# Kernel tuning notes

Measured on AMD Instinct MI355X. Metric: run time of the kernel, lower is better.

The kernel has to match this reference:

```python
import jax, jax.numpy as jnp
import numpy as np
from jax import lax

G, N0, E, P = 50, 1000, 4000, 10          # graphs, nodes/graph, edges/graph, patients
FEAT, NHID, GDIM, RATIO = 1036, 128, 32, 0.2
NLAYERS = 3


def setup_inputs():
    key = jax.random.key(0)
    ks = jax.random.split(key, 32)
    x = jax.random.uniform(ks[0], (G * N0, FEAT), jnp.float32)
    off = (jnp.arange(G) * N0)[:, None]
    src = jax.random.randint(ks[1], (G, E), 0, N0) + off
    dst = jax.random.randint(ks[2], (G, E), 0, N0) + off
    edge_index = jnp.stack([src.reshape(-1), dst.reshape(-1)]).astype(jnp.int32)
    graphs_per_pat = jnp.full((P,), G // P, jnp.int32)

    def lin(k, i, o):
        return jax.random.normal(k, (i, o), jnp.float32) / np.float32(np.sqrt(i))

    d = {"x": x, "edge_index": edge_index, "graphs_per_pat": graphs_per_pat}
    ins = [FEAT, NHID, NHID]
    ki = 3
    for l in range(NLAYERS):
        d[f"c{l}_wl"] = lin(ks[ki], ins[l], NHID)
        d[f"c{l}_bl"] = jnp.zeros(NHID, jnp.float32)
        d[f"c{l}_wr"] = lin(ks[ki + 1], ins[l], NHID)
        d[f"p{l}_wrel"] = lin(ks[ki + 2], NHID, 1)
        d[f"p{l}_brel"] = jnp.zeros(1, jnp.float32)
        d[f"p{l}_wroot"] = lin(ks[ki + 3], NHID, 1)
        ki += 4
    d["lin1_w"] = lin(ks[ki], 2 * NHID, NHID); d["lin1_b"] = jnp.zeros(NHID, jnp.float32)
    d["lin2_w"] = lin(ks[ki + 1], NHID, GDIM); d["lin2_b"] = jnp.zeros(GDIM, jnp.float32)
    d["grade_w"] = lin(ks[ki + 2], GDIM, 3); d["grade_b"] = jnp.zeros(3, jnp.float32)
    d["haz_w"] = lin(ks[ki + 3], GDIM, 1); d["haz_b"] = jnp.zeros(1, jnp.float32)
    return d


def _sage(x, src, dst, m, wl, bl, wr, M):
    # PyG SAGEConv, mean aggregation: out = lin_l(mean_j x_j) + lin_r(x_i)
    agg = jax.ops.segment_sum(x[src] * m[:, None], dst, num_segments=M)
    cnt = jax.ops.segment_sum(m, dst, num_segments=M)
    mean = agg / jnp.maximum(cnt, 1.0)[:, None]
    return mean @ wl + bl + x @ wr


def _sag_pool(x, src, dst, m, wrel, brel, wroot, n, k):
    # SAGPooling: GraphConv (add aggr) score -> per-graph top-k -> tanh gate -> edge filter
    M = G * n
    agg = jax.ops.segment_sum(x[src] * m[:, None], dst, num_segments=M)
    score = (agg @ wrel + brel + x @ wroot).reshape(G, n)  # [G, n]
    _, idx = lax.top_k(score, k)                            # [G, k]
    sel = jnp.take_along_axis(score, idx, axis=1)           # [G, k]
    perm = (idx + (jnp.arange(G) * n)[:, None]).reshape(-1)
    nx = x[perm] * jnp.tanh(sel).reshape(-1, 1)             # [G*k, NHID]
    mapping = jnp.full((M,), -1, jnp.int32).at[perm].set(jnp.arange(G * k, dtype=jnp.int32))
    ns, nd = mapping[src], mapping[dst]
    nm = m * (ns >= 0) * (nd >= 0)                          # keep edge iff both endpoints survive
    return nx, jnp.maximum(ns, 0), jnp.maximum(nd, 0), nm


def _forward(x, edge_index, graphs_per_pat, params):
    # normalize_graphs: first 12 feature columns divided by their column max
    x = jnp.concatenate([x[:, :12] / jnp.max(x[:, :12], axis=0, keepdims=True), x[:, 12:]], axis=1)
    src, dst = edge_index[0], edge_index[1]
    m = jnp.ones(src.shape[0], x.dtype)
    n = N0
    xs = []
    for l in range(NLAYERS):
        k = int(np.ceil(RATIO * n))
        x = jax.nn.relu(_sage(x, src, dst, m, params[f"c{l}_wl"], params[f"c{l}_bl"], params[f"c{l}_wr"], G * n))
        x, src, dst, m = _sag_pool(x, src, dst, m, params[f"p{l}_wrel"], params[f"p{l}_brel"], params[f"p{l}_wroot"], n, k)
        n = k
        xr = x.reshape(G, n, NHID)
        xs.append(jnp.concatenate([xr.max(axis=1), xr.mean(axis=1)], axis=1))  # [G, 2*NHID]
    h = xs[0] + xs[1] + xs[2]
    # patient-level mean pool
    bv = jnp.repeat(jnp.arange(P), graphs_per_pat, total_repeat_length=G)
    pooled = jax.ops.segment_sum(h, bv, num_segments=P) / graphs_per_pat[:, None].astype(h.dtype)
    h = jax.nn.relu(pooled @ params["lin1_w"] + params["lin1_b"])  # dropout omitted (deterministic ref)
    feats = jax.nn.relu(h @ params["lin2_w"] + params["lin2_b"])
    grade = jax.nn.log_softmax(feats @ params["grade_w"] + params["grade_b"], axis=1)
    hazard = jax.nn.sigmoid(feats @ params["haz_w"] + params["haz_b"]) * 6.0 - 3.0
    return feats, grade, hazard


def reference(x, edge_index, graphs_per_pat,
              c0_wl, c0_bl, c0_wr, p0_wrel, p0_brel, p0_wroot,
              c1_wl, c1_bl, c1_wr, p1_wrel, p1_brel, p1_wroot,
              c2_wl, c2_bl, c2_wr, p2_wrel, p2_brel, p2_wroot,
              lin1_w, lin1_b, lin2_w, lin2_b, grade_w, grade_b, haz_w, haz_b):
    params = dict(
        c0_wl=c0_wl, c0_bl=c0_bl, c0_wr=c0_wr, p0_wrel=p0_wrel, p0_brel=p0_brel, p0_wroot=p0_wroot,
        c1_wl=c1_wl, c1_bl=c1_bl, c1_wr=c1_wr, p1_wrel=p1_wrel, p1_brel=p1_brel, p1_wroot=p1_wroot,
        c2_wl=c2_wl, c2_bl=c2_bl, c2_wr=c2_wr, p2_wrel=p2_wrel, p2_brel=p2_brel, p2_wroot=p2_wroot,
        lin1_w=lin1_w, lin1_b=lin1_b, lin2_w=lin2_w, lin2_b=lin2_b,
        grade_w=grade_w, grade_b=grade_b, haz_w=haz_w, haz_b=haz_b)
    return _forward(x, edge_index, graphs_per_pat, params)
```

## Files before the change

### kernel.cpp

```cpp
#include <hip/hip_runtime.h>
#include <math.h>
#include <cfloat>

#define G_    50
#define N0_   1000
#define NEDGE 200000
#define EPG_  (NEDGE/G_)
#define P_    10
#define FEAT_ 1036
#define NHID_ 128
#define GDIM_ 32
#define K0_   200
#define K1_   40
#define K2_   8
#define M0_   (G_*N0_)
#define M1_   (G_*K0_)
#define M2_   (G_*K1_)

#define KPAD_ 1088
#define MPAD0_ 50048
#define MPAD1_ 10112
#define MPAD2_ 2048

typedef __attribute__((ext_vector_type(8))) short s16x8;
typedef __attribute__((ext_vector_type(4))) float f32x4;

__device__ __forceinline__ unsigned f2bf1(float f) {
  unsigned u = __float_as_uint(f);
  return (u + 0x7FFFu + ((u >> 16) & 1u)) >> 16;
}
__device__ __forceinline__ unsigned packbf(float a, float b) {
  return f2bf1(a) | (f2bf1(b) << 16);
}

__device__ __forceinline__ void gload_lds16(const void* g, void* l) {
  __builtin_amdgcn_global_load_lds((const __attribute__((address_space(1))) void*)g,
                                   (__attribute__((address_space(3))) void*)l, 16, 0, 0);
}


__global__ void colmax_kernel(const float* __restrict__ x, int* __restrict__ scale_i) {
  int tid = threadIdx.x, wave = tid >> 6, lane = tid & 63;
  float mx[12];
#pragma unroll
  for (int j = 0; j < 12; j++) mx[j] = 0.f;
  for (int r = blockIdx.x * 256 + tid; r < M0_; r += gridDim.x * 256) {
    const float4* p = (const float4*)(x + (size_t)r * FEAT_);
    float4 a = p[0], b = p[1], c = p[2];
    mx[0] = fmaxf(mx[0], a.x); mx[1] = fmaxf(mx[1], a.y);
    mx[2] = fmaxf(mx[2], a.z); mx[3] = fmaxf(mx[3], a.w);
    mx[4] = fmaxf(mx[4], b.x); mx[5] = fmaxf(mx[5], b.y);
    mx[6] = fmaxf(mx[6], b.z); mx[7] = fmaxf(mx[7], b.w);
    mx[8] = fmaxf(mx[8], c.x); mx[9] = fmaxf(mx[9], c.y);
    mx[10] = fmaxf(mx[10], c.z); mx[11] = fmaxf(mx[11], c.w);
  }
#pragma unroll
  for (int off = 32; off > 0; off >>= 1)
#pragma unroll
    for (int j = 0; j < 12; j++) mx[j] = fmaxf(mx[j], __shfl_down(mx[j], off));
  __shared__ float red[4][12];
  if (lane == 0)
#pragma unroll
    for (int j = 0; j < 12; j++) red[wave][j] = mx[j];
  __syncthreads();
  if (tid < 12) {
    float m = fmaxf(fmaxf(red[0][tid], red[1][tid]), fmaxf(red[2][tid], red[3][tid]));
    atomicMax(scale_i + tid, __float_as_int(m));
  }
}

__global__ void build_wt0_kernel(const float* __restrict__ wl, const float* __restrict__ wr,
                                 const int* __restrict__ scale_i, unsigned short* __restrict__ WT) {
  int idx = blockIdx.x * blockDim.x + threadIdx.x;
  if (idx >= 256 * KPAD_) return;
  int c = idx / KPAD_, j = idx % KPAD_;
  float w = 0.f;
  if (j < FEAT_) {
    w = (c < NHID_) ? wl[j * NHID_ + c] : wr[j * NHID_ + (c - NHID_)];
    if (j < 12) w *= 1.0f / __int_as_float(scale_i[j]);
  }
  WT[idx] = (unsigned short)f2bf1(w);
}

__global__ void build_wt12_kernel(const float* __restrict__ wl1, const float* __restrict__ wr1,
                                  const float* __restrict__ wl2, const float* __restrict__ wr2,
                                  unsigned short* __restrict__ WTA, unsigned short* __restrict__ WTB) {
  int idx = blockIdx.x * blockDim.x + threadIdx.x;
  if (idx >= 2 * 256 * 128) return;
  int l = idx >> 15, r = idx & 32767;
  int c = r >> 7, j = r & 127;
  const float* wl = l ? wl2 : wl1;
  const float* wr = l ? wr2 : wr1;
  float w = (c < NHID_) ? wl[j * NHID_ + c] : wr[j * NHID_ + (c - NHID_)];
  (l ? WTB : WTA)[r] = (unsigned short)f2bf1(w);
}

template <bool AF32>
__global__ __launch_bounds__(256) void mfma_gemm_kernel(const float* __restrict__ Af,
                                                        const unsigned short* __restrict__ Ab,
                                                        const unsigned short* __restrict__ WT,
                                                        float* __restrict__ C, int M,
                                                        int lda, int ldb, int kvalid, int ksteps) {
  __shared__ unsigned short As[2 * 128 * 32];
  __shared__ unsigned short Bs[2 * 256 * 32];
  const int bm = blockIdx.x * 128;
  const int tid = threadIdx.x, wave = tid >> 6, lane = tid & 63;
  const int wr = wave >> 1, wc = wave & 1;
  const int lhi = lane >> 4, llo = lane & 15;
  const int arow = tid >> 1, ahalf = tid & 1;
  f32x4 acc[4][8] = {};

  for (int st = 0; st < ksteps; st++) {
    const int k0 = st * 64;
#pragma unroll
    for (int it = 0; it < 8; it++) {
      int c = it * 256 + wave * 64 + lane;
      int kk = c >> 10, r = (c >> 2) & 255, cb = c & 3;
      gload_lds16(WT + (size_t)r * ldb + k0 + kk * 32 + cb * 8, Bs + (size_t)c * 8);
    }
    {
      int gr = bm + arow;
      int gk = k0 + ahalf * 32;
      unsigned short* dstp = As + ahalf * 4096 + arow * 32;
      if (AF32) {
        float f[32];
        if (gr < M && gk + 32 <= kvalid) {
          const float4* ap = (const float4*)(Af + (size_t)gr * lda + gk);
#pragma unroll
          for (int j = 0; j < 8; j++) {
            float4 v = ap[j];
            f[4 * j] = v.x; f[4 * j + 1] = v.y; f[4 * j + 2] = v.z; f[4 * j + 3] = v.w;
          }
        } else {
          const float* ap = Af + (size_t)gr * lda + gk;
#pragma unroll
          for (int j = 0; j < 32; j++)
            f[j] = (gr < M && gk + j < kvalid) ? ap[j] : 0.f;
        }
#pragma unroll
        for (int j = 0; j < 4; j++) {
          uint4 p;
          p.x = packbf(f[8 * j + 0], f[8 * j + 1]); p.y = packbf(f[8 * j + 2], f[8 * j + 3]);
          p.z = packbf(f[8 * j + 4], f[8 * j + 5]); p.w = packbf(f[8 * j + 6], f[8 * j + 7]);
          *(uint4*)(dstp + j * 8) = p;
        }
      } else {
        const uint4* ap = (const uint4*)(Ab + (size_t)gr * lda + gk);
#pragma unroll
        for (int j = 0; j < 4; j++) ((uint4*)dstp)[j] = ap[j];
      }
    }
    __syncthreads();

#pragma unroll
    for (int kk = 0; kk < 2; kk++) {
      s16x8 a[4], b[8];
#pragma unroll
      for (int mt = 0; mt < 4; mt++)
        a[mt] = *(const s16x8*)&As[kk * 4096 + (wr * 64 + mt * 16 + llo) * 32 + lhi * 8];
#pragma unroll
      for (int nt = 0; nt < 8; nt++)
        b[nt] = *(const s16x8*)&Bs[kk * 8192 + (wc * 128 + nt * 16 + llo) * 32 + lhi * 8];
#pragma unroll
      for (int mt = 0; mt < 4; mt++)
#pragma unroll
        for (int nt = 0; nt < 8; nt++)
          acc[mt][nt] = __builtin_amdgcn_mfma_f32_16x16x32_bf16(a[mt], b[nt], acc[mt][nt], 0, 0, 0);
    }
    __syncthreads();
  }

#pragma unroll
  for (int mt = 0; mt < 4; mt++) {
#pragma unroll
    for (int q = 0; q < 4; q++) {
      int row = bm + wr * 64 + mt * 16 + lhi * 4 + q;
      if (row < M) {
#pragma unroll
        for (int nt = 0; nt < 8; nt++)
          C[(size_t)row * 256 + wc * 128 + nt * 16 + llo] = acc[mt][nt][q];
      }
    }
  }
}

__global__ __launch_bounds__(1024) void csr_graph_kernel(const int* __restrict__ src,
                                                         const int* __restrict__ dst,
                                                         const float* __restrict__ m, int n,
                                                         int* __restrict__ deg,
                                                         int* __restrict__ offs,
                                                         int* __restrict__ eid) {
  __shared__ int sdeg[1024];
  __shared__ int soff[1024];
  __shared__ int scur[1024];
  __shared__ int spart[1024];
  const int g = blockIdx.x, tid = threadIdx.x;
  sdeg[tid] = 0;
  __syncthreads();
  const int e0 = g * EPG_;
  for (int e = tid; e < EPG_; e += 1024) {
    int ge = e0 + e;
    if (!m || m[ge] != 0.f) atomicAdd(&sdeg[dst[ge] - g * n], 1);
  }
  __syncthreads();
  int v = (tid < n) ? sdeg[tid] : 0;
  spart[tid] = v;
  __syncthreads();
  for (int ofs = 1; ofs < 1024; ofs <<= 1) {
    int t = (tid >= ofs) ? spart[tid - ofs] : 0;
    __syncthreads();
    spart[tid] += t;
    __syncthreads();
  }
  if (tid < n) {
    soff[tid] = spart[tid] - sdeg[tid];
    scur[tid] = 0;
    deg[g * n + tid] = sdeg[tid];
    offs[g * n + tid] = g * EPG_ + soff[tid];
  }
  __syncthreads();
  for (int e = tid; e < EPG_; e += 1024) {
    int ge = e0 + e;
    if (!m || m[ge] != 0.f) {
      int d = dst[ge] - g * n;
      int p = atomicAdd(&scur[d], 1);
      eid[g * EPG_ + soff[d] + p] = src[ge];
    }
  }
}

__global__ void agg_sage_dots_kernel(const float* __restrict__ Y,
                                     const int* __restrict__ eid, const int* __restrict__ offs,
                                     const int* __restrict__ deg,
                                     const float* __restrict__ bl,
                                     const float* __restrict__ wrel, const float* __restrict__ wroot,
                                     float* __restrict__ X, float* __restrict__ T,
                                     float* __restrict__ R, int M) {
  int wid = threadIdx.x >> 6, lane = threadIdx.x & 63;
  int i = blockIdx.x * 4 + wid;
  if (i >= M) return;
  int d = deg[i], o = offs[i];
  float a0 = 0.f, a1 = 0.f;
  for (int j = 0; j < d; j++) {
    int s = eid[o + j];
    a0 += Y[(size_t)s * 256 + lane];
    a1 += Y[(size_t)s * 256 + 64 + lane];
  }
  float ic = 1.f / fmaxf((float)d, 1.f);
  float v0 = a0 * ic + bl[lane] + Y[(size_t)i * 256 + 128 + lane];
  float v1 = a1 * ic + bl[64 + lane] + Y[(size_t)i * 256 + 192 + lane];
  v0 = fmaxf(v0, 0.f); v1 = fmaxf(v1, 0.f);
  X[(size_t)i * 128 + lane] = v0;
  X[(size_t)i * 128 + 64 + lane] = v1;
  float t = v0 * wrel[lane] + v1 * wrel[64 + lane];
  float r = v0 * wroot[lane] + v1 * wroot[64 + lane];
#pragma unroll
  for (int off = 32; off > 0; off >>= 1) {
    t += __shfl_down(t, off);
    r += __shfl_down(r, off);
  }
  if (lane == 0) { T[i] = t; R[i] = r; }
}

template <int NP>
__global__ __launch_bounds__(1024) void pool_kernel(
    const float* __restrict__ X, const float* __restrict__ T, const float* __restrict__ R,
    const float* __restrict__ brel,
    const int* __restrict__ src, const int* __restrict__ dst, const float* __restrict__ m,
    const int* __restrict__ deg, const int* __restrict__ offs, const int* __restrict__ eid,
    int n, int k,
    unsigned short* __restrict__ NXB,
    int* __restrict__ nsrc, int* __restrict__ ndst, float* __restrict__ nm,
    float* __restrict__ H) {
  __shared__ float val[NP];
  __shared__ int   ind[256];
  __shared__ int   lmap[NP];
  __shared__ float gate[256];
  __shared__ float redmx[8][128];
  __shared__ float redsm[8][128];
  const int g = blockIdx.x, tid = threadIdx.x, nthr = blockDim.x;
  float b0 = brel[0];
  for (int i = tid; i < n; i += nthr) {
    int gi = g * n + i;
    int dd = deg[gi], o = offs[gi];
    float s = 0.f;
    for (int j = 0; j < dd; j++) s += T[eid[o + j]];
    val[i] = s + R[gi] + b0;
    lmap[i] = -1;
  }
  __syncthreads();
  for (int i = tid; i < n; i += nthr) {
    float vi = val[i];
    int rank = 0;
    for (int j = 0; j < n; j++) {
      float vj = val[j];
      rank += (vj > vi) || (vj == vi && j < i);
    }
    if (rank < k) {
      lmap[i] = rank;
      ind[rank] = i;
      gate[rank] = tanhf(vi);
    }
  }
  __syncthreads();
  for (int idx = tid; idx < k * 128; idx += nthr) {
    int t = idx >> 7, c = idx & 127;
    float v = X[(size_t)(g * n + ind[t]) * 128 + c] * gate[t];
    NXB[(size_t)(g * k + t) * 128 + c] = (unsigned short)f2bf1(v);
  }
  {
    int c = tid & 127, seg = tid >> 7;
    float mxv = -FLT_MAX, smv = 0.f;
    for (int t = seg; t < k; t += 8) {
      float v = X[(size_t)(g * n + ind[t]) * 128 + c] * gate[t];
      mxv = fmaxf(mxv, v);
      smv += v;
    }
    redmx[seg][c] = mxv;
    redsm[seg][c] = smv;
  }
  __syncthreads();
  if (tid < 128) {
    float Mv = redmx[0][tid], S = redsm[0][tid];
#pragma unroll
    for (int s2 = 1; s2 < 8; s2++) { Mv = fmaxf(Mv, redmx[s2][tid]); S += redsm[s2][tid]; }
    H[g * 256 + tid] += Mv;
    H[g * 256 + 128 + tid] += S / (float)k;
  }
  if (nsrc) {
    const int e0 = g * EPG_;
    for (int e = tid; e < EPG_; e += nthr) {
      int ge = e0 + e;
      int ls = lmap[src[ge] - g * n], ld = lmap[dst[ge] - g * n];
      float me = m ? m[ge] : 1.f;
      nm[ge] = (ls >= 0 && ld >= 0) ? me : 0.f;
      nsrc[ge] = g * k + max(ls, 0);
      ndst[ge] = g * k + max(ld, 0);
    }
  }
}

__global__ void head_kernel(const float* __restrict__ H, const int* __restrict__ gpp,
                            const float* __restrict__ lin1_w, const float* __restrict__ lin1_b,
                            const float* __restrict__ lin2_w, const float* __restrict__ lin2_b,
                            const float* __restrict__ grade_w, const float* __restrict__ grade_b,
                            const float* __restrict__ haz_w, const float* __restrict__ haz_b,
                            float* __restrict__ out) {
  __shared__ float pooled[P_][256];
  __shared__ float h1[P_][NHID_];
  __shared__ float feats[P_][GDIM_];
  __shared__ int off[P_ + 1];
  int tid = threadIdx.x;
  if (tid == 0) {
    off[0] = 0;
    for (int p = 0; p < P_; p++) off[p + 1] = min(off[p] + gpp[p], G_);
  }
  __syncthreads();
  for (int idx = tid; idx < P_ * 256; idx += blockDim.x) {
    int p = idx >> 8, c = idx & 255;
    int a = off[p], b = (p == P_ - 1) ? G_ : off[p + 1];
    float s = 0.f;
    for (int gq = a; gq < b; gq++) s += H[gq * 256 + c];
    pooled[p][c] = s / (float)gpp[p];
  }
  __syncthreads();
  for (int idx = tid; idx < P_ * NHID_; idx += blockDim.x) {
    int p = idx >> 7, o = idx & 127;
    float acc = lin1_b[o];
    for (int c = 0; c < 256; c++) acc += pooled[p][c] * lin1_w[c * NHID_ + o];
    h1[p][o] = fmaxf(acc, 0.f);
  }
  __syncthreads();
  for (int idx = tid; idx < P_ * GDIM_; idx += blockDim.x) {
    int p = idx / GDIM_, o = idx % GDIM_;
    float acc = lin2_b[o];
    for (int c = 0; c < NHID_; c++) acc += h1[p][c] * lin2_w[c * GDIM_ + o];
    float f = fmaxf(acc, 0.f);
    feats[p][o] = f;
    out[p * GDIM_ + o] = f;
  }
  __syncthreads();
  if (tid < P_) {
    int p = tid;
    float l[3];
    float mx = -FLT_MAX;
    for (int j = 0; j < 3; j++) {
      float acc = grade_b[j];
      for (int c = 0; c < GDIM_; c++) acc += feats[p][c] * grade_w[c * 3 + j];
      l[j] = acc;
      mx = fmaxf(mx, acc);
    }
    float se = 0.f;
    for (int j = 0; j < 3; j++) se += expf(l[j] - mx);
    float lse = mx + logf(se);
    for (int j = 0; j < 3; j++) out[P_ * GDIM_ + p * 3 + j] = l[j] - lse;
    float z = haz_b[0];
    for (int c = 0; c < GDIM_; c++) z += feats[p][c] * haz_w[c];
    out[P_ * GDIM_ + P_ * 3 + p] = 6.f / (1.f + expf(-z)) - 3.f;
  }
}

extern "C" void kernel_launch(void* const* d_in, const int* in_sizes, int n_in,
                              void* d_out, int out_size, void* d_ws, size_t ws_size,
                              hipStream_t stream) {
  (void)in_sizes; (void)n_in; (void)out_size; (void)ws_size;
  const float* x  = (const float*)d_in[0];
  const int* ei   = (const int*)d_in[1];
  const int* gpp  = (const int*)d_in[2];
  const float* c_wl[3]    = {(const float*)d_in[3],  (const float*)d_in[9],  (const float*)d_in[15]};
  const float* c_bl[3]    = {(const float*)d_in[4],  (const float*)d_in[10], (const float*)d_in[16]};
  const float* c_wr[3]    = {(const float*)d_in[5],  (const float*)d_in[11], (const float*)d_in[17]};
  const float* p_wrel[3]  = {(const float*)d_in[6],  (const float*)d_in[12], (const float*)d_in[18]};
  const float* p_brel[3]  = {(const float*)d_in[7],  (const float*)d_in[13], (const float*)d_in[19]};
  const float* p_wroot[3] = {(const float*)d_in[8],  (const float*)d_in[14], (const float*)d_in[20]};
  const float* lin1_w = (const float*)d_in[21];
  const float* lin1_b = (const float*)d_in[22];
  const float* lin2_w = (const float*)d_in[23];
  const float* lin2_b = (const float*)d_in[24];
  const float* grade_w = (const float*)d_in[25];
  const float* grade_b = (const float*)d_in[26];
  const float* haz_w = (const float*)d_in[27];
  const float* haz_b = (const float*)d_in[28];

  char* wsb = (char*)d_ws;
  size_t off = 0;
  auto alloc = [&](size_t bytes) -> void* {
    void* p = wsb + off;
    off += (bytes + 255) & ~(size_t)255;
    return p;
  };
  int*            SCALE = (int*)alloc(64 * 4);
  unsigned short* WT0   = (unsigned short*)alloc((size_t)256 * KPAD_ * 2);
  unsigned short* WT1   = (unsigned short*)alloc((size_t)256 * 128 * 2);
  unsigned short* WT2   = (unsigned short*)alloc((size_t)256 * 128 * 2);
  float*          YZ    = (float*)alloc((size_t)M0_ * 256 * 4);
  float*          H     = (float*)alloc((size_t)G_ * 256 * 4);
  float* X     = (float*)alloc((size_t)M0_ * 128 * 4);
  unsigned short* NXB = (unsigned short*)alloc((size_t)MPAD1_ * 128 * 2);
  float* T     = (float*)alloc((size_t)M0_ * 4);
  float* R     = (float*)alloc((size_t)M0_ * 4);
  int*   DEG   = (int*)alloc((size_t)M0_ * 4);
  int*   OFF   = (int*)alloc((size_t)M0_ * 4);
  int*   EID   = (int*)alloc((size_t)NEDGE * 4);
  int*   E1S   = (int*)alloc((size_t)NEDGE * 4);
  int*   E1D   = (int*)alloc((size_t)NEDGE * 4);
  float* E1M   = (float*)alloc((size_t)NEDGE * 4);
  int*   E2S   = (int*)alloc((size_t)NEDGE * 4);
  int*   E2D   = (int*)alloc((size_t)NEDGE * 4);
  float* E2M   = (float*)alloc((size_t)NEDGE * 4);

  const int* src0 = ei;
  const int* dst0 = ei + NEDGE;

  hipMemsetAsync(H, 0, G_ * 256 * sizeof(float), stream);
  hipMemsetAsync(SCALE, 0, 12 * sizeof(int), stream);

  colmax_kernel<<<128, 256, 0, stream>>>(x, SCALE);
  build_wt0_kernel<<<(256 * KPAD_ + 255) / 256, 256, 0, stream>>>(c_wl[0], c_wr[0], SCALE, WT0);
  build_wt12_kernel<<<(2 * 256 * 128 + 255) / 256, 256, 0, stream>>>(c_wl[1], c_wr[1], c_wl[2], c_wr[2], WT1, WT2);

  csr_graph_kernel<<<G_, 1024, 0, stream>>>(src0, dst0, nullptr, N0_, DEG, OFF, EID);
  mfma_gemm_kernel<true><<<MPAD0_ / 128, 256, 0, stream>>>(x, nullptr, WT0, YZ, M0_, FEAT_, KPAD_, FEAT_, KPAD_ / 64);
  agg_sage_dots_kernel<<<(M0_ + 3) / 4, 256, 0, stream>>>(YZ, EID, OFF, DEG, c_bl[0], p_wrel[0], p_wroot[0], X, T, R, M0_);
  pool_kernel<1024><<<G_, 1024, 0, stream>>>(X, T, R, p_brel[0], src0, dst0, nullptr,
                                             DEG, OFF, EID, N0_, K0_, NXB, E1S, E1D, E1M, H);

  csr_graph_kernel<<<G_, 1024, 0, stream>>>(E1S, E1D, E1M, K0_, DEG, OFF, EID);
  mfma_gemm_kernel<false><<<MPAD1_ / 128, 256, 0, stream>>>(nullptr, NXB, WT1, YZ, M1_, 128, 128, 128, 2);
  agg_sage_dots_kernel<<<(M1_ + 3) / 4, 256, 0, stream>>>(YZ, EID, OFF, DEG, c_bl[1], p_wrel[1], p_wroot[1], X, T, R, M1_);
  pool_kernel<256><<<G_, 1024, 0, stream>>>(X, T, R, p_brel[1], E1S, E1D, E1M,
                                            DEG, OFF, EID, K0_, K1_, NXB, E2S, E2D, E2M, H);

  csr_graph_kernel<<<G_, 1024, 0, stream>>>(E2S, E2D, E2M, K1_, DEG, OFF, EID);
  mfma_gemm_kernel<false><<<MPAD2_ / 128, 256, 0, stream>>>(nullptr, NXB, WT2, YZ, M2_, 128, 128, 128, 2);
  agg_sage_dots_kernel<<<(M2_ + 3) / 4, 256, 0, stream>>>(YZ, EID, OFF, DEG, c_bl[2], p_wrel[2], p_wroot[2], X, T, R, M2_);
  pool_kernel<64><<<G_, 1024, 0, stream>>>(X, T, R, p_brel[2], E2S, E2D, E2M,
                                           DEG, OFF, EID, K1_, K2_, NXB, nullptr, nullptr, nullptr, H);

  head_kernel<<<1, 256, 0, stream>>>(H, gpp, lin1_w, lin1_b, lin2_w, lin2_b,
                                     grade_w, grade_b, haz_w, haz_b, (float*)d_out);
}
```

Measured before the change: 300.6 us.

## Double-buffer GEMM B tiles and build pooled-graph CSR directly in pool kernel

The MFMA GEMM now prefetches the next K-step's A rows into registers and its B tile into a second LDS buffer while the current step computes, overlapping global loads with matrix math at the cost of more LDS and registers plus an extra barrier. The pool kernel also builds the filtered CSR adjacency (degree, offsets, neighbor ids) for the next layer straight from the current CSR, so the per-layer csr_graph launches and the edge-list/mask arrays are removed. The CSR prefix sum is done serially by one thread and neighbor order may differ, which can slightly change float summation order.

```diff
diff --git a/kernel.cpp b/kernel.cpp
--- a/kernel.cpp
+++ b/kernel.cpp
@@ -102,7 +102,7 @@
                                                         float* __restrict__ C, int M,
                                                         int lda, int ldb, int kvalid, int ksteps) {
   __shared__ unsigned short As[2 * 128 * 32];
-  __shared__ unsigned short Bs[2 * 256 * 32];
+  __shared__ unsigned short Bs[2][2 * 256 * 32];
   const int bm = blockIdx.x * 128;
   const int tid = threadIdx.x, wave = tid >> 6, lane = tid & 63;
   const int wr = wave >> 1, wc = wave & 1;
@@ -110,48 +110,70 @@
   const int arow = tid >> 1, ahalf = tid & 1;
   f32x4 acc[4][8] = {};
 
-  for (int st = 0; st < ksteps; st++) {
+  float fA[32];
+  uint4 vA[4];
+
+  auto loadA = [&](int st) {
+    const int k0 = st * 64;
+    int gr = bm + arow;
+    int gk = k0 + ahalf * 32;
+    if (AF32) {
+      if (gr < M && gk + 32 <= kvalid) {
+        const float4* ap = (const float4*)(Af + (size_t)gr * lda + gk);
+#pragma unroll
+        for (int j = 0; j < 8; j++) {
+          float4 v = ap[j];
+          fA[4 * j] = v.x; fA[4 * j + 1] = v.y; fA[4 * j + 2] = v.z; fA[4 * j + 3] = v.w;
+        }
+      } else {
+        const float* ap = Af + (size_t)gr * lda + gk;
+#pragma unroll
+        for (int j = 0; j < 32; j++)
+          fA[j] = (gr < M && gk + j < kvalid) ? ap[j] : 0.f;
+      }
+    } else {
+      const uint4* ap = (const uint4*)(Ab + (size_t)gr * lda + gk);
+#pragma unroll
+      for (int j = 0; j < 4; j++) vA[j] = ap[j];
+    }
+  };
+  auto writeA = [&]() {
+    unsigned short* dstp = As + ahalf * 4096 + arow * 32;
+    if (AF32) {
+#pragma unroll
+      for (int j = 0; j < 4; j++) {
+        uint4 p;
+        p.x = packbf(fA[8 * j + 0], fA[8 * j + 1]); p.y = packbf(fA[8 * j + 2], fA[8 * j + 3]);
+        p.z = packbf(fA[8 * j + 4], fA[8 * j + 5]); p.w = packbf(fA[8 * j + 6], fA[8 * j + 7]);
+        *(uint4*)(dstp + j * 8) = p;
+      }
+    } else {
+#pragma unroll
+      for (int j = 0; j < 4; j++) ((uint4*)dstp)[j] = vA[j];
+    }
+  };
+  auto stageB = [&](int st, int b) {
     const int k0 = st * 64;
 #pragma unroll
     for (int it = 0; it < 8; it++) {
       int c = it * 256 + wave * 64 + lane;
       int kk = c >> 10, r = (c >> 2) & 255, cb = c & 3;
-      gload_lds16(WT + (size_t)r * ldb + k0 + kk * 32 + cb * 8, Bs + (size_t)c * 8);
-    }
-    {
-      int gr = bm + arow;
-      int gk = k0 + ahalf * 32;
-      unsigned short* dstp = As + ahalf * 4096 + arow * 32;
-      if (AF32) {
-        float f[32];
-        if (gr < M && gk + 32 <= kvalid) {
-          const float4* ap = (const float4*)(Af + (size_t)gr * lda + gk);
-#pragma unroll
-          for (int j = 0; j < 8; j++) {
-            float4 v = ap[j];
-            f[4 * j] = v.x; f[4 * j + 1] = v.y; f[4 * j + 2] = v.z; f[4 * j + 3] = v.w;
-          }
-        } else {
-          const float* ap = Af + (size_t)gr * lda + gk;
-#pragma unroll
-          for (int j = 0; j < 32; j++)
-            f[j] = (gr < M && gk + j < kvalid) ? ap[j] : 0.f;
-        }
-#pragma unroll
-        for (int j = 0; j < 4; j++) {
-          uint4 p;
-          p.x = packbf(f[8 * j + 0], f[8 * j + 1]); p.y = packbf(f[8 * j + 2], f[8 * j + 3]);
-          p.z = packbf(f[8 * j + 4], f[8 * j + 5]); p.w = packbf(f[8 * j + 6], f[8 * j + 7]);
-          *(uint4*)(dstp + j * 8) = p;
-        }
-      } else {
-        const uint4* ap = (const uint4*)(Ab + (size_t)gr * lda + gk);
-#pragma unroll
-        for (int j = 0; j < 4; j++) ((uint4*)dstp)[j] = ap[j];
-      }
-    }
-    __syncthreads();
-
+      gload_lds16(WT + (size_t)r * ldb + k0 + kk * 32 + cb * 8, &Bs[b][(size_t)c * 8]);
+    }
+  };
+
+  loadA(0);
+  stageB(0, 0);
+  writeA();
+  __syncthreads();
+
+  for (int st = 0; st < ksteps; st++) {
+    const int bbuf = st & 1;
+    const bool more = (st + 1 < ksteps);
+    if (more) {
+      loadA(st + 1);
+      stageB(st + 1, bbuf ^ 1);
+    }
 #pragma unroll
     for (int kk = 0; kk < 2; kk++) {
       s16x8 a[4], b[8];
@@ -160,14 +182,18 @@
         a[mt] = *(const s16x8*)&As[kk * 4096 + (wr * 64 + mt * 16 + llo) * 32 + lhi * 8];
 #pragma unroll
       for (int nt = 0; nt < 8; nt++)
-        b[nt] = *(const s16x8*)&Bs[kk * 8192 + (wc * 128 + nt * 16 + llo) * 32 + lhi * 8];
+        b[nt] = *(const s16x8*)&Bs[bbuf][kk * 8192 + (wc * 128 + nt * 16 + llo) * 32 + lhi * 8];
 #pragma unroll
       for (int mt = 0; mt < 4; mt++)
 #pragma unroll
         for (int nt = 0; nt < 8; nt++)
           acc[mt][nt] = __builtin_amdgcn_mfma_f32_16x16x32_bf16(a[mt], b[nt], acc[mt][nt], 0, 0, 0);
     }
-    __syncthreads();
+    if (more) {
+      __syncthreads();
+      writeA();
+      __syncthreads();
+    }
   }
 
 #pragma unroll
@@ -186,7 +212,7 @@
 
 __global__ __launch_bounds__(1024) void csr_graph_kernel(const int* __restrict__ src,
                                                          const int* __restrict__ dst,
-                                                         const float* __restrict__ m, int n,
+                                                         int n,
                                                          int* __restrict__ deg,
                                                          int* __restrict__ offs,
                                                          int* __restrict__ eid) {
@@ -198,10 +224,8 @@
   sdeg[tid] = 0;
   __syncthreads();
   const int e0 = g * EPG_;
-  for (int e = tid; e < EPG_; e += 1024) {
-    int ge = e0 + e;
-    if (!m || m[ge] != 0.f) atomicAdd(&sdeg[dst[ge] - g * n], 1);
-  }
+  for (int e = tid; e < EPG_; e += 1024)
+    atomicAdd(&sdeg[dst[e0 + e] - g * n], 1);
   __syncthreads();
   int v = (tid < n) ? sdeg[tid] : 0;
   spart[tid] = v;
@@ -221,11 +245,9 @@
   __syncthreads();
   for (int e = tid; e < EPG_; e += 1024) {
     int ge = e0 + e;
-    if (!m || m[ge] != 0.f) {
-      int d = dst[ge] - g * n;
-      int p = atomicAdd(&scur[d], 1);
-      eid[g * EPG_ + soff[d] + p] = src[ge];
-    }
+    int d = dst[ge] - g * n;
+    int p = atomicAdd(&scur[d], 1);
+    eid[g * EPG_ + soff[d] + p] = src[ge];
   }
 }
 
@@ -266,16 +288,17 @@
 __global__ __launch_bounds__(1024) void pool_kernel(
     const float* __restrict__ X, const float* __restrict__ T, const float* __restrict__ R,
     const float* __restrict__ brel,
-    const int* __restrict__ src, const int* __restrict__ dst, const float* __restrict__ m,
     const int* __restrict__ deg, const int* __restrict__ offs, const int* __restrict__ eid,
     int n, int k,
     unsigned short* __restrict__ NXB,
-    int* __restrict__ nsrc, int* __restrict__ ndst, float* __restrict__ nm,
+    int* __restrict__ degN, int* __restrict__ offsN, int* __restrict__ eidN,
     float* __restrict__ H) {
   __shared__ float val[NP];
   __shared__ int   ind[256];
   __shared__ int   lmap[NP];
   __shared__ float gate[256];
+  __shared__ int   sdegN[256];
+  __shared__ int   soffN[256];
   __shared__ float redmx[8][128];
   __shared__ float redsm[8][128];
   const int g = blockIdx.x, tid = threadIdx.x, nthr = blockDim.x;
@@ -327,15 +350,35 @@
     H[g * 256 + tid] += Mv;
     H[g * 256 + 128 + tid] += S / (float)k;
   }
-  if (nsrc) {
-    const int e0 = g * EPG_;
-    for (int e = tid; e < EPG_; e += nthr) {
-      int ge = e0 + e;
-      int ls = lmap[src[ge] - g * n], ld = lmap[dst[ge] - g * n];
-      float me = m ? m[ge] : 1.f;
-      nm[ge] = (ls >= 0 && ld >= 0) ? me : 0.f;
-      nsrc[ge] = g * k + max(ls, 0);
-      ndst[ge] = g * k + max(ld, 0);
+  if (degN) {
+    for (int t = tid; t < k; t += nthr) sdegN[t] = 0;
+    __syncthreads();
+    for (int d = tid; d < n; d += nthr) {
+      int ld = lmap[d];
+      if (ld < 0) continue;
+      int gd = g * n + d, dd = deg[gd], o = offs[gd];
+      int cnt = 0;
+      for (int j = 0; j < dd; j++)
+        cnt += (lmap[eid[o + j] - g * n] >= 0);
+      sdegN[ld] = cnt;
+    }
+    __syncthreads();
+    if (tid == 0) {
+      int run = 0;
+      for (int t = 0; t < k; t++) { soffN[t] = run; run += sdegN[t]; }
+    }
+    __syncthreads();
+    for (int d = tid; d < n; d += nthr) {
+      int ld = lmap[d];
+      if (ld < 0) continue;
+      int gd = g * n + d, dd = deg[gd], o = offs[gd];
+      int p = 0;
+      for (int j = 0; j < dd; j++) {
+        int ls = lmap[eid[o + j] - g * n];
+        if (ls >= 0) eidN[g * EPG_ + soffN[ld] + (p++)] = g * k + ls;
+      }
+      degN[g * k + ld] = p;
+      offsN[g * k + ld] = g * EPG_ + soffN[ld];
     }
   }
 }
@@ -439,15 +482,12 @@
   unsigned short* NXB = (unsigned short*)alloc((size_t)MPAD1_ * 128 * 2);
   float* T     = (float*)alloc((size_t)M0_ * 4);
   float* R     = (float*)alloc((size_t)M0_ * 4);
-  int*   DEG   = (int*)alloc((size_t)M0_ * 4);
-  int*   OFF   = (int*)alloc((size_t)M0_ * 4);
-  int*   EID   = (int*)alloc((size_t)NEDGE * 4);
-  int*   E1S   = (int*)alloc((size_t)NEDGE * 4);
-  int*   E1D   = (int*)alloc((size_t)NEDGE * 4);
-  float* E1M   = (float*)alloc((size_t)NEDGE * 4);
-  int*   E2S   = (int*)alloc((size_t)NEDGE * 4);
-  int*   E2D   = (int*)alloc((size_t)NEDGE * 4);
-  float* E2M   = (float*)alloc((size_t)NEDGE * 4);
+  int*   DEG0  = (int*)alloc((size_t)M0_ * 4);
+  int*   OFF0  = (int*)alloc((size_t)M0_ * 4);
+  int*   EID0  = (int*)alloc((size_t)NEDGE * 4);
+  int*   DEG1  = (int*)alloc((size_t)M1_ * 4);
+  int*   OFF1  = (int*)alloc((size_t)M1_ * 4);
+  int*   EID1  = (int*)alloc((size_t)NEDGE * 4);
 
   const int* src0 = ei;
   const int* dst0 = ei + NEDGE;
@@ -459,23 +499,21 @@
   build_wt0_kernel<<<(256 * KPAD_ + 255) / 256, 256, 0, stream>>>(c_wl[0], c_wr[0], SCALE, WT0);
   build_wt12_kernel<<<(2 * 256 * 128 + 255) / 256, 256, 0, stream>>>(c_wl[1], c_wr[1], c_wl[2], c_wr[2], WT1, WT2);
 
-  csr_graph_kernel<<<G_, 1024, 0, stream>>>(src0, dst0, nullptr, N0_, DEG, OFF, EID);
+  csr_graph_kernel<<<G_, 1024, 0, stream>>>(src0, dst0, N0_, DEG0, OFF0, EID0);
   mfma_gemm_kernel<true><<<MPAD0_ / 128, 256, 0, stream>>>(x, nullptr, WT0, YZ, M0_, FEAT_, KPAD_, FEAT_, KPAD_ / 64);
-  agg_sage_dots_kernel<<<(M0_ + 3) / 4, 256, 0, stream>>>(YZ, EID, OFF, DEG, c_bl[0], p_wrel[0], p_wroot[0], X, T, R, M0_);
-  pool_kernel<1024><<<G_, 1024, 0, stream>>>(X, T, R, p_brel[0], src0, dst0, nullptr,
-                                             DEG, OFF, EID, N0_, K0_, NXB, E1S, E1D, E1M, H);
-
-  csr_graph_kernel<<<G_, 1024, 0, stream>>>(E1S, E1D, E1M, K0_, DEG, OFF, EID);
+  agg_sage_dots_kernel<<<(M0_ + 3) / 4, 256, 0, stream>>>(YZ, EID0, OFF0, DEG0, c_bl[0], p_wrel[0], p_wroot[0], X, T, R, M0_);
+  pool_kernel<1024><<<G_, 1024, 0, stream>>>(X, T, R, p_brel[0], DEG0, OFF0, EID0,
+                                             N0_, K0_, NXB, DEG1, OFF1, EID1, H);
+
   mfma_gemm_kernel<false><<<MPAD1_ / 128, 256, 0, stream>>>(nullptr, NXB, WT1, YZ, M1_, 128, 128, 128, 2);
-  agg_sage_dots_kernel<<<(M1_ + 3) / 4, 256, 0, stream>>>(YZ, EID, OFF, DEG, c_bl[1], p_wrel[1], p_wroot[1], X, T, R, M1_);
-  pool_kernel<256><<<G_, 1024, 0, stream>>>(X, T, R, p_brel[1], E1S, E1D, E1M,
-                                            DEG, OFF, EID, K0_, K1_, NXB, E2S, E2D, E2M, H);
-
-  csr_graph_kernel<<<G_, 1024, 0, stream>>>(E2S, E2D, E2M, K1_, DEG, OFF, EID);
+  agg_sage_dots_kernel<<<(M1_ + 3) / 4, 256, 0, stream>>>(YZ, EID1, OFF1, DEG1, c_bl[1], p_wrel[1], p_wroot[1], X, T, R, M1_);
+  pool_kernel<256><<<G_, 1024, 0, stream>>>(X, T, R, p_brel[1], DEG1, OFF1, EID1,
+                                            K0_, K1_, NXB, DEG0, OFF0, EID0, H);
+
   mfma_gemm_kernel<false><<<MPAD2_ / 128, 256, 0, stream>>>(nullptr, NXB, WT2, YZ, M2_, 128, 128, 128, 2);
-  agg_sage_dots_kernel<<<(M2_ + 3) / 4, 256, 0, stream>>>(YZ, EID, OFF, DEG, c_bl[2], p_wrel[2], p_wroot[2], X, T, R, M2_);
-  pool_kernel<64><<<G_, 1024, 0, stream>>>(X, T, R, p_brel[2], E2S, E2D, E2M,
-                                           DEG, OFF, EID, K1_, K2_, NXB, nullptr, nullptr, nullptr, H);
+  agg_sage_dots_kernel<<<(M2_ + 3) / 4, 256, 0, stream>>>(YZ, EID0, OFF0, DEG0, c_bl[2], p_wrel[2], p_wroot[2], X, T, R, M2_);
+  pool_kernel<64><<<G_, 1024, 0, stream>>>(X, T, R, p_brel[2], DEG0, OFF0, EID0,
+                                           K1_, K2_, NXB, nullptr, nullptr, nullptr, H);
 
   head_kernel<<<1, 256, 0, stream>>>(H, gpp, lin1_w, lin1_b, lin2_w, lin2_b,
                                      grade_w, grade_b, haz_w, haz_b, (float*)d_out);
```

After: 335.3 us. 1.12x slower.
